# Performance work log

Hardware: AMD Instinct MI355X
Metric: run time of the kernel (lower is better)

The kernel has to match this reference:

```python
import jax, jax.numpy as jnp
import numpy as np

NUM_FT = 40960      # HalfKP feature count
NUM_FFT = 640       # factorized feature count
FT_OUT = 256        # feature transformer width
MAX_FEATURES = 32   # max active features per position


def _embed_sum(w, b, idx, vals):
    # w: [V, D], idx: [B, F] int, vals: [B, F] -> [B, D]
    # bias + weighted sum of gathered embedding rows
    return b + jnp.einsum('bf,bfd->bd', vals, w[idx])


def setup_inputs() -> dict:
    key = jax.random.key(0)
    ks = jax.random.split(key, 9)
    B = 8192
    values = jax.random.uniform(ks[0], (B, MAX_FEATURES), dtype=jnp.float32)
    stm_indices = jax.random.randint(ks[1], (B, MAX_FEATURES), 0, NUM_FT, dtype=jnp.int32)
    nstm_indices = jax.random.randint(ks[2], (B, MAX_FEATURES), 0, NUM_FT, dtype=jnp.int32)
    s = 0.02
    ft_w = jax.random.normal(ks[3], (NUM_FT, FT_OUT), dtype=jnp.float32) * s
    ft_b = jax.random.normal(ks[4], (FT_OUT,), dtype=jnp.float32) * s
    fft_w = jax.random.normal(ks[5], (NUM_FFT, FT_OUT), dtype=jnp.float32) * s
    fft_b = jax.random.normal(ks[6], (FT_OUT,), dtype=jnp.float32) * s
    out_w = jax.random.normal(ks[7], (1, 2 * FT_OUT), dtype=jnp.float32) * s
    out_b = jax.random.normal(ks[8], (1,), dtype=jnp.float32) * s
    return {"values": values, "stm_indices": stm_indices, "nstm_indices": nstm_indices,
            "ft_w": ft_w, "ft_b": ft_b, "fft_w": fft_w, "fft_b": fft_b,
            "out_w": out_w, "out_b": out_b}


def reference(values, stm_indices, nstm_indices, ft_w, ft_b, fft_w, fft_b, out_w, out_b):
    stm_ft = _embed_sum(ft_w, ft_b, stm_indices, values)
    nstm_ft = _embed_sum(ft_w, ft_b, nstm_indices, values)
    v_stm_ft = _embed_sum(fft_w, fft_b, stm_indices % NUM_FFT, values)
    v_nstm_ft = _embed_sum(fft_w, fft_b, nstm_indices % NUM_FFT, values)
    hidden = jnp.clip(jnp.concatenate([stm_ft + v_stm_ft, nstm_ft + v_nstm_ft], axis=1), 0.0, 1.0)
    return jax.nn.sigmoid(hidden @ out_w.T + out_b)
```

## Files before the change

### kernel.cpp

```cpp
#include <hip/hip_runtime.h>
#include <math.h>

constexpr int kMaxF   = 32;
constexpr int kFtOut  = 256;
constexpr int kNumFFT = 640;
constexpr int kNumFT  = 40960;

__device__ __forceinline__ float clip01(float x) {
    return fminf(fmaxf(x, 0.0f), 1.0f);
}

__device__ __forceinline__ unsigned short f2bf(float x) {
    unsigned int u = __float_as_uint(x);
    unsigned int r = (u + 0x7fffu + ((u >> 16) & 1u)) >> 16;
    return (unsigned short)r;
}

__global__ __launch_bounds__(256) void prep_comb_kernel(
    const float* __restrict__ ft_w,
    const float* __restrict__ fft_w,
    unsigned short* __restrict__ comb,
    int total4)
{
    const int t = blockIdx.x * blockDim.x + threadIdx.x;
    if (t >= total4) return;
    const int elem = t << 2;
    const int row  = elem >> 8;
    const int d    = elem & (kFtOut - 1);
    const float4 a = *reinterpret_cast<const float4*>(ft_w + elem);
    const float4 b = *reinterpret_cast<const float4*>(fft_w + (row % kNumFFT) * kFtOut + d);
    ushort4 o;
    o.x = f2bf(a.x + b.x);
    o.y = f2bf(a.y + b.y);
    o.z = f2bf(a.z + b.z);
    o.w = f2bf(a.w + b.w);
    *reinterpret_cast<ushort4*>(comb + elem) = o;
}

__global__ __launch_bounds__(256) void nnue_comb_kernel(
    const float* __restrict__ values,
    const int*   __restrict__ stm_idx,
    const int*   __restrict__ nstm_idx,
    const float* __restrict__ ft_b,
    const float* __restrict__ fft_b,
    const unsigned short* __restrict__ comb,
    const float* __restrict__ out_w,
    const float* __restrict__ out_b,
    float*       __restrict__ out,
    int batch)
{
    const int gtid = blockIdx.x * blockDim.x + threadIdx.x;
    const int b    = gtid >> 6;
    const int lane = threadIdx.x & 63;
    if (b >= batch) return;

    float v_reg = 0.0f;
    int   i_reg = 0;
    if (lane < kMaxF) {
        v_reg = values[b * kMaxF + lane];
        i_reg = stm_idx[b * kMaxF + lane];
    } else {
        i_reg = nstm_idx[b * kMaxF + (lane - kMaxF)];
    }

    const int dbase = (lane & 31) * 8;

    float acc[8];
    {
        const float4 b0 = *reinterpret_cast<const float4*>(ft_b + dbase);
        const float4 b1 = *reinterpret_cast<const float4*>(ft_b + dbase + 4);
        const float4 c0 = *reinterpret_cast<const float4*>(fft_b + dbase);
        const float4 c1 = *reinterpret_cast<const float4*>(fft_b + dbase + 4);
        acc[0] = b0.x + c0.x; acc[1] = b0.y + c0.y; acc[2] = b0.z + c0.z; acc[3] = b0.w + c0.w;
        acc[4] = b1.x + c1.x; acc[5] = b1.y + c1.y; acc[6] = b1.z + c1.z; acc[7] = b1.w + c1.w;
    }

    const int side_sel = lane & 32;

#pragma unroll 8
    for (int f = 0; f < kMaxF; ++f) {
        const float v   = __shfl(v_reg, f, 64);
        const int   idx = __shfl(i_reg, f + side_sel, 64);
        const uint4 raw = *reinterpret_cast<const uint4*>(comb + idx * kFtOut + dbase);
        const float w0 = __uint_as_float(raw.x << 16);
        const float w1 = __uint_as_float(raw.x & 0xffff0000u);
        const float w2 = __uint_as_float(raw.y << 16);
        const float w3 = __uint_as_float(raw.y & 0xffff0000u);
        const float w4 = __uint_as_float(raw.z << 16);
        const float w5 = __uint_as_float(raw.z & 0xffff0000u);
        const float w6 = __uint_as_float(raw.w << 16);
        const float w7 = __uint_as_float(raw.w & 0xffff0000u);
        acc[0] = fmaf(v, w0, acc[0]);
        acc[1] = fmaf(v, w1, acc[1]);
        acc[2] = fmaf(v, w2, acc[2]);
        acc[3] = fmaf(v, w3, acc[3]);
        acc[4] = fmaf(v, w4, acc[4]);
        acc[5] = fmaf(v, w5, acc[5]);
        acc[6] = fmaf(v, w6, acc[6]);
        acc[7] = fmaf(v, w7, acc[7]);
    }

    const float4 ow0 = *reinterpret_cast<const float4*>(out_w + 8 * lane);
    const float4 ow1 = *reinterpret_cast<const float4*>(out_w + 8 * lane + 4);

    float p = clip01(acc[0]) * ow0.x + clip01(acc[1]) * ow0.y
            + clip01(acc[2]) * ow0.z + clip01(acc[3]) * ow0.w
            + clip01(acc[4]) * ow1.x + clip01(acc[5]) * ow1.y
            + clip01(acc[6]) * ow1.z + clip01(acc[7]) * ow1.w;

#pragma unroll
    for (int off = 32; off > 0; off >>= 1)
        p += __shfl_down(p, off, 64);

    if (lane == 0) {
        const float x = p + out_b[0];
        out[b] = 1.0f / (1.0f + expf(-x));
    }
}

__device__ __forceinline__ void fma4(float4& acc, float v, const float4& a, const float4& b) {
    acc.x = fmaf(v, a.x + b.x, acc.x);
    acc.y = fmaf(v, a.y + b.y, acc.y);
    acc.z = fmaf(v, a.z + b.z, acc.z);
    acc.w = fmaf(v, a.w + b.w, acc.w);
}

__global__ __launch_bounds__(256) void nnue_halfkp_fallback(
    const float* __restrict__ values,
    const int*   __restrict__ stm_idx,
    const int*   __restrict__ nstm_idx,
    const float* __restrict__ ft_w,
    const float* __restrict__ ft_b,
    const float* __restrict__ fft_w,
    const float* __restrict__ fft_b,
    const float* __restrict__ out_w,
    const float* __restrict__ out_b,
    float*       __restrict__ out,
    int batch)
{
    const int gtid = blockIdx.x * blockDim.x + threadIdx.x;
    const int b    = gtid >> 6;
    const int lane = threadIdx.x & 63;
    if (b >= batch) return;

    float v_reg = 0.0f;
    int   i_reg = 0;
    if (lane < kMaxF) {
        v_reg = values[b * kMaxF + lane];
        i_reg = stm_idx[b * kMaxF + lane];
    } else {
        i_reg = nstm_idx[b * kMaxF + (lane - kMaxF)];
    }

    const float4* ftw4  = reinterpret_cast<const float4*>(ft_w);
    const float4* fftw4 = reinterpret_cast<const float4*>(fft_w);

    const float4 fb  = reinterpret_cast<const float4*>(ft_b)[lane];
    const float4 ffb = reinterpret_cast<const float4*>(fft_b)[lane];
    float4 acc_s = make_float4(fb.x + ffb.x, fb.y + ffb.y, fb.z + ffb.z, fb.w + ffb.w);
    float4 acc_n = acc_s;

#pragma unroll 8
    for (int f = 0; f < kMaxF; ++f) {
        const float v  = __shfl(v_reg, f, 64);
        const int   is = __shfl(i_reg, f, 64);
        const int   in = __shfl(i_reg, f + kMaxF, 64);
        const float4 as = ftw4[is * 64 + lane];
        const float4 bs = fftw4[(is % kNumFFT) * 64 + lane];
        const float4 an = ftw4[in * 64 + lane];
        const float4 bn = fftw4[(in % kNumFFT) * 64 + lane];
        fma4(acc_s, v, as, bs);
        fma4(acc_n, v, an, bn);
    }

    const float4* ow4 = reinterpret_cast<const float4*>(out_w);
    const float4 ws = ow4[lane];
    const float4 wn = ow4[64 + lane];

    float p = clip01(acc_s.x) * ws.x + clip01(acc_s.y) * ws.y
            + clip01(acc_s.z) * ws.z + clip01(acc_s.w) * ws.w
            + clip01(acc_n.x) * wn.x + clip01(acc_n.y) * wn.y
            + clip01(acc_n.z) * wn.z + clip01(acc_n.w) * wn.w;

#pragma unroll
    for (int off = 32; off > 0; off >>= 1)
        p += __shfl_down(p, off, 64);

    if (lane == 0) {
        const float x = p + out_b[0];
        out[b] = 1.0f / (1.0f + expf(-x));
    }
}

extern "C" void kernel_launch(void* const* d_in, const int* in_sizes, int n_in,
                              void* d_out, int out_size, void* d_ws, size_t ws_size,
                              hipStream_t stream) {
    const float* values = (const float*)d_in[0];
    const int*   stm    = (const int*)  d_in[1];
    const int*   nstm   = (const int*)  d_in[2];
    const float* ft_w   = (const float*)d_in[3];
    const float* ft_b   = (const float*)d_in[4];
    const float* fft_w  = (const float*)d_in[5];
    const float* fft_b  = (const float*)d_in[6];
    const float* out_w  = (const float*)d_in[7];
    const float* out_b  = (const float*)d_in[8];
    float* out = (float*)d_out;

    const int batch = in_sizes[0] / kMaxF;
    const size_t comb_bytes = (size_t)kNumFT * kFtOut * sizeof(unsigned short);

    if (ws_size >= comb_bytes) {
        unsigned short* comb = (unsigned short*)d_ws;
        const int total4 = kNumFT * kFtOut / 4;
        hipLaunchKernelGGL(prep_comb_kernel, dim3((total4 + 255) / 256), dim3(256), 0, stream,
                           ft_w, fft_w, comb, total4);
        const int blocks = (batch * 64 + 255) / 256;
        hipLaunchKernelGGL(nnue_comb_kernel, dim3(blocks), dim3(256), 0, stream,
                           values, stm, nstm, ft_b, fft_b, comb, out_w, out_b, out, batch);
    } else {
        const int blocks = (batch * 64 + 255) / 256;
        hipLaunchKernelGGL(nnue_halfkp_fallback, dim3(blocks), dim3(256), 0, stream,
                           values, stm, nstm, ft_w, ft_b, fft_w, fft_b, out_w, out_b, out, batch);
    }
}
```

Before: 130.5 us.

## Quantize combined feature table to int8 with per-row scales

Replaces the bf16 combined weight table with an int8 table plus one float scale per row, built by a prep kernel that does a wave-wide max reduction per row. The main kernel folds the row scale into the feature value before the loop and gathers 8 bytes per lane instead of 16, halving gather traffic. The prep kernel also writes half as many bytes. This loses precision compared to bf16 (about 7 bits per weight relative to the row max), which risks exceeding accuracy tolerances. The loop unroll is also raised.

```diff
diff --git a/kernel.cpp b/kernel.cpp
--- a/kernel.cpp
+++ b/kernel.cpp
@@ -10,40 +10,51 @@
     return fminf(fmaxf(x, 0.0f), 1.0f);
 }
 
-__device__ __forceinline__ unsigned short f2bf(float x) {
-    unsigned int u = __float_as_uint(x);
-    unsigned int r = (u + 0x7fffu + ((u >> 16) & 1u)) >> 16;
-    return (unsigned short)r;
-}
-
-__global__ __launch_bounds__(256) void prep_comb_kernel(
+__global__ __launch_bounds__(256) void prep_q8_kernel(
     const float* __restrict__ ft_w,
     const float* __restrict__ fft_w,
-    unsigned short* __restrict__ comb,
-    int total4)
+    signed char* __restrict__ qtab,
+    float*       __restrict__ scales,
+    int rows)
 {
-    const int t = blockIdx.x * blockDim.x + threadIdx.x;
-    if (t >= total4) return;
-    const int elem = t << 2;
-    const int row  = elem >> 8;
-    const int d    = elem & (kFtOut - 1);
-    const float4 a = *reinterpret_cast<const float4*>(ft_w + elem);
-    const float4 b = *reinterpret_cast<const float4*>(fft_w + (row % kNumFFT) * kFtOut + d);
-    ushort4 o;
-    o.x = f2bf(a.x + b.x);
-    o.y = f2bf(a.y + b.y);
-    o.z = f2bf(a.z + b.z);
-    o.w = f2bf(a.w + b.w);
-    *reinterpret_cast<ushort4*>(comb + elem) = o;
-}
-
-__global__ __launch_bounds__(256) void nnue_comb_kernel(
+    const int wid  = (blockIdx.x * blockDim.x + threadIdx.x) >> 6;
+    const int lane = threadIdx.x & 63;
+    if (wid >= rows) return;
+    const int d = lane * 4;
+    const float4 a = *reinterpret_cast<const float4*>(ft_w + wid * kFtOut + d);
+    const float4 c = *reinterpret_cast<const float4*>(fft_w + (wid % kNumFFT) * kFtOut + d);
+    const float w0 = a.x + c.x, w1 = a.y + c.y, w2 = a.z + c.z, w3 = a.w + c.w;
+
+    float m = fmaxf(fmaxf(fabsf(w0), fabsf(w1)), fmaxf(fabsf(w2), fabsf(w3)));
+#pragma unroll
+    for (int off = 32; off > 0; off >>= 1)
+        m = fmaxf(m, __shfl_xor(m, off, 64));
+
+    const float s_inv = (m > 0.0f) ? 127.0f / m : 0.0f;
+    int q0 = (int)rintf(w0 * s_inv);
+    int q1 = (int)rintf(w1 * s_inv);
+    int q2 = (int)rintf(w2 * s_inv);
+    int q3 = (int)rintf(w3 * s_inv);
+    q0 = min(max(q0, -127), 127);
+    q1 = min(max(q1, -127), 127);
+    q2 = min(max(q2, -127), 127);
+    q3 = min(max(q3, -127), 127);
+    const unsigned int pack = (unsigned int)(q0 & 0xff)
+                            | ((unsigned int)(q1 & 0xff) << 8)
+                            | ((unsigned int)(q2 & 0xff) << 16)
+                            | ((unsigned int)(q3 & 0xff) << 24);
+    *reinterpret_cast<unsigned int*>(qtab + (size_t)wid * kFtOut + d) = pack;
+    if (lane == 0) scales[wid] = (m > 0.0f) ? m / 127.0f : 0.0f;
+}
+
+__global__ __launch_bounds__(256) void nnue_q8_kernel(
     const float* __restrict__ values,
     const int*   __restrict__ stm_idx,
     const int*   __restrict__ nstm_idx,
     const float* __restrict__ ft_b,
     const float* __restrict__ fft_b,
-    const unsigned short* __restrict__ comb,
+    const signed char* __restrict__ qtab,
+    const float* __restrict__ scales,
     const float* __restrict__ out_w,
     const float* __restrict__ out_b,
     float*       __restrict__ out,
@@ -63,7 +74,11 @@
         i_reg = nstm_idx[b * kMaxF + (lane - kMaxF)];
     }
 
-    const int dbase = (lane & 31) * 8;
+    const float v_full = __shfl(v_reg, lane & 31, 64);
+    const float vp     = v_full * scales[i_reg];
+
+    const int dbase    = (lane & 31) * 8;
+    const int side_sel = lane & 32;
 
     float acc[8];
     {
@@ -75,29 +90,20 @@
         acc[4] = b1.x + c1.x; acc[5] = b1.y + c1.y; acc[6] = b1.z + c1.z; acc[7] = b1.w + c1.w;
     }
 
-    const int side_sel = lane & 32;
-
-#pragma unroll 8
+#pragma unroll 16
     for (int f = 0; f < kMaxF; ++f) {
-        const float v   = __shfl(v_reg, f, 64);
+        const float vs  = __shfl(vp,    f + side_sel, 64);
         const int   idx = __shfl(i_reg, f + side_sel, 64);
-        const uint4 raw = *reinterpret_cast<const uint4*>(comb + idx * kFtOut + dbase);
-        const float w0 = __uint_as_float(raw.x << 16);
-        const float w1 = __uint_as_float(raw.x & 0xffff0000u);
-        const float w2 = __uint_as_float(raw.y << 16);
-        const float w3 = __uint_as_float(raw.y & 0xffff0000u);
-        const float w4 = __uint_as_float(raw.z << 16);
-        const float w5 = __uint_as_float(raw.z & 0xffff0000u);
-        const float w6 = __uint_as_float(raw.w << 16);
-        const float w7 = __uint_as_float(raw.w & 0xffff0000u);
-        acc[0] = fmaf(v, w0, acc[0]);
-        acc[1] = fmaf(v, w1, acc[1]);
-        acc[2] = fmaf(v, w2, acc[2]);
-        acc[3] = fmaf(v, w3, acc[3]);
-        acc[4] = fmaf(v, w4, acc[4]);
-        acc[5] = fmaf(v, w5, acc[5]);
-        acc[6] = fmaf(v, w6, acc[6]);
-        acc[7] = fmaf(v, w7, acc[7]);
+        const int2 raw = *reinterpret_cast<const int2*>(qtab + (size_t)idx * kFtOut + dbase);
+        const int x = raw.x, y = raw.y;
+        acc[0] = fmaf(vs, (float)((x << 24) >> 24), acc[0]);
+        acc[1] = fmaf(vs, (float)((x << 16) >> 24), acc[1]);
+        acc[2] = fmaf(vs, (float)((x <<  8) >> 24), acc[2]);
+        acc[3] = fmaf(vs, (float)( x        >> 24), acc[3]);
+        acc[4] = fmaf(vs, (float)((y << 24) >> 24), acc[4]);
+        acc[5] = fmaf(vs, (float)((y << 16) >> 24), acc[5]);
+        acc[6] = fmaf(vs, (float)((y <<  8) >> 24), acc[6]);
+        acc[7] = fmaf(vs, (float)( y        >> 24), acc[7]);
     }
 
     const float4 ow0 = *reinterpret_cast<const float4*>(out_w + 8 * lane);
@@ -207,16 +213,18 @@
     float* out = (float*)d_out;
 
     const int batch = in_sizes[0] / kMaxF;
-    const size_t comb_bytes = (size_t)kNumFT * kFtOut * sizeof(unsigned short);
-
-    if (ws_size >= comb_bytes) {
-        unsigned short* comb = (unsigned short*)d_ws;
-        const int total4 = kNumFT * kFtOut / 4;
-        hipLaunchKernelGGL(prep_comb_kernel, dim3((total4 + 255) / 256), dim3(256), 0, stream,
-                           ft_w, fft_w, comb, total4);
+    const size_t qtab_bytes  = (size_t)kNumFT * kFtOut;
+    const size_t scale_bytes = (size_t)kNumFT * sizeof(float);
+
+    if (ws_size >= qtab_bytes + scale_bytes) {
+        signed char* qtab = (signed char*)d_ws;
+        float* scales = (float*)((char*)d_ws + qtab_bytes);
+        const int prep_blocks = (kNumFT * 64 + 255) / 256;
+        hipLaunchKernelGGL(prep_q8_kernel, dim3(prep_blocks), dim3(256), 0, stream,
+                           ft_w, fft_w, qtab, scales, kNumFT);
         const int blocks = (batch * 64 + 255) / 256;
-        hipLaunchKernelGGL(nnue_comb_kernel, dim3(blocks), dim3(256), 0, stream,
-                           values, stm, nstm, ft_b, fft_b, comb, out_w, out_b, out, batch);
+        hipLaunchKernelGGL(nnue_q8_kernel, dim3(blocks), dim3(256), 0, stream,
+                           values, stm, nstm, ft_b, fft_b, qtab, scales, out_w, out_b, out, batch);
     } else {
         const int blocks = (batch * 64 + 255) / 256;
         hipLaunchKernelGGL(nnue_halfkp_fallback, dim3(blocks), dim3(256), 0, stream,
```

Result: faster. 115.6 us (-11.4%).
